# Optimization experiments

Measured on AMD Instinct MI355X. Metric: run time of the kernel, lower is better.

Reference implementation:

```python
import jax, jax.numpy as jnp
import numpy as np
from jax import lax

IN_CH, FEAT, EMB, P = 384, 256, 32, 64
OUT_CH = (256, 512, 1024, 1024)
EPS_BN = 1e-5


def _conv(x, w, b, stride=1, pad=1, groups=1):
    # x: (B,C,H,W), w: (O, C//groups, kh, kw) torch OIHW layout
    y = lax.conv_general_dilated(x, w, (stride, stride), ((pad, pad), (pad, pad)),
                                 dimension_numbers=('NCHW', 'OIHW', 'NCHW'),
                                 feature_group_count=groups)
    return y + b[None, :, None, None]


def _bn(x, g, b, m, v):
    scale = (g / jnp.sqrt(v + EPS_BN))[None, :, None, None]
    return (x - m[None, :, None, None]) * scale + b[None, :, None, None]


def _convT_block(x, w, b, k):
    # ConvTranspose2d with kernel_size == stride == k, padding 0 (non-overlapping)
    # w: (C_in, C_out, k, k) torch layout
    B, C, H, W = x.shape
    O = w.shape[1]
    y = jnp.einsum('bchw,coij->bohiwj', x, w).reshape(B, O, H * k, W * k)
    return y + b[None, :, None, None]


def _resize_ac(x, oh, ow):
    # bilinear interpolation, align_corners=True; x: (B,C,H,W)
    H, W = x.shape[-2], x.shape[-1]
    def idx(n_in, n_out):
        c = jnp.arange(n_out, dtype=x.dtype) * ((n_in - 1) / max(n_out - 1, 1))
        i0 = jnp.clip(jnp.floor(c).astype(jnp.int32), 0, max(n_in - 2, 0))
        return i0, c - i0.astype(x.dtype)
    if oh != H:
        i0, t = idx(H, oh)
        x = x[:, :, i0, :] * (1.0 - t)[:, None] + x[:, :, jnp.minimum(i0 + 1, H - 1), :] * t[:, None]
    if ow != W:
        j0, t = idx(W, ow)
        x = x[:, :, :, j0] * (1.0 - t) + x[:, :, :, jnp.minimum(j0 + 1, W - 1)] * t
    return x


def _avg3(x):
    # F.avg_pool2d(k=3, s=1, p=1) with count_include_pad=True -> always /9
    s = lax.reduce_window(x, jnp.float32(0.0), lax.add, (1, 1, 3, 3), (1, 1, 1, 1),
                          ((0, 0), (0, 0), (1, 1), (1, 1)))
    return s / 9.0


def _forward(tokens0, tokens1, tokens2, tokens3,
             proj_w0, proj_b0, proj_w1, proj_b1, proj_w2, proj_b2, proj_w3, proj_b3,
             up_w0, up_b0, up_w1, up_b1, down_w3, down_b3,
             fuse_w, fuse_b,
             pe_w1, pe_b1, pe_bn_g, pe_bn_b, pe_bn_m, pe_bn_v, pe_w2, pe_b2,
             prototypes, prototype_biases, bias_scale,
             smooth_w, smooth_b,
             head_w1, head_b1, hbn1_g, hbn1_b, hbn1_m, hbn1_v,
             head_w2, head_b2, hbn2_g, hbn2_b, hbn2_m, hbn2_v,
             head_w3, head_b3, residual_scale,
             patch_h, patch_w):
    B = tokens0.shape[0]
    toks = (tokens0, tokens1, tokens2, tokens3)
    proj = ((proj_w0, proj_b0), (proj_w1, proj_b1), (proj_w2, proj_b2), (proj_w3, proj_b3))
    feats = []
    for t, (w, b) in zip(toks, proj):
        x = t.transpose(0, 2, 1).reshape(B, t.shape[-1], patch_h, patch_w)
        x = jnp.einsum('bchw,oc->bohw', x, w[:, :, 0, 0]) + b[None, :, None, None]  # 1x1 proj
        feats.append(x)
    f0 = _convT_block(feats[0], up_w0, up_b0, 4)
    f1 = _convT_block(feats[1], up_w1, up_b1, 2)
    f2 = feats[2]                                         # identity
    f3 = _conv(feats[3], down_w3, down_b3, stride=2)
    th, tw = f0.shape[-2], f0.shape[-1]
    fused = jnp.concatenate([f0, _resize_ac(f1, th, tw), _resize_ac(f2, th, tw), _resize_ac(f3, th, tw)], axis=1)
    path1 = jax.nn.relu(jnp.einsum('bchw,oc->bohw', fused, fuse_w[:, :, 0, 0]) + fuse_b[None, :, None, None])
    H, W = patch_h * 14, patch_w * 14
    path1 = _resize_ac(path1, H, W)
    pe = _conv(path1, pe_w1, pe_b1)
    pe = jax.nn.relu(_bn(pe, pe_bn_g, pe_bn_b, pe_bn_m, pe_bn_v))
    pe = _conv(pe, pe_w2, pe_b2)                          # (B, EMB, H, W)
    sim = jnp.einsum('behw,pe->bphw', pe, prototypes) / jnp.sqrt(jnp.float32(pe.shape[1]))
    # edge map from embedding gradients, replicate-padded
    gx = jnp.abs(pe[:, :, :, :-1] - pe[:, :, :, 1:])
    gy = jnp.abs(pe[:, :, :-1, :] - pe[:, :, 1:, :])
    gx = jnp.concatenate([gx, gx[:, :, :, -1:]], axis=3)
    gy = jnp.concatenate([gy, gy[:, :, -1:, :]], axis=2)
    edge = (gx.mean(axis=1, keepdims=True) + gy.mean(axis=1, keepdims=True)) * 0.5
    mask = (edge > edge.mean()).astype(pe.dtype)
    for _ in range(2):  # fixed 2-step edge-aware smoothing
        sim = mask * sim + (1.0 - mask) * _avg3(sim)
    # first softmax over prototypes -> entropy regularizer
    act1 = jax.nn.softmax(sim, axis=1)
    activation_entropy = -(act1 * jnp.log(act1 + 1e-8)).sum(axis=1).mean()
    # spatial smoothing conv then second softmax over prototypes
    sim = _conv(sim, smooth_w, smooth_b)
    act = jax.nn.softmax(sim, axis=1)                     # (B, P, H, W)
    bb = 1.0 + jnp.tanh(prototype_biases) * bias_scale    # (P,)
    base_biases = jnp.broadcast_to(bb[None, :], (B, bb.shape[0]))
    base_gain = jnp.einsum('bphw,p->bhw', act, bb)[:, None]  # (B,1,H,W)
    # 64 per-prototype residual heads == grouped convs with groups=P
    n_proto = act.shape[1]
    h = jax.nn.relu(_bn(_conv(act, head_w1, head_b1, groups=n_proto), hbn1_g, hbn1_b, hbn1_m, hbn1_v))
    h = jax.nn.relu(_bn(_conv(h, head_w2, head_b2, groups=n_proto), hbn2_g, hbn2_b, hbn2_m, hbn2_v))
    res = _conv(h, head_w3, head_b3, groups=n_proto)      # (B, P, H, W)
    weighted = (act * res).sum(axis=1, keepdims=True)
    gain = base_gain * (1.0 + jnp.tanh(weighted) * residual_scale)
    instance_bias_map = jnp.clip(gain, 0.5, 2.0)
    return instance_bias_map, act, base_biases, weighted, pe, activation_entropy


def setup_inputs() -> dict:
    key = jax.random.key(0)
    B, N, PH, PW = 2, 256, 16, 16
    ks = iter(jax.random.split(key, 48))
    def rnd(shape, s=1.0):
        return jax.random.normal(next(ks), shape, dtype=jnp.float32) * s
    inp = {}
    for i in range(4):
        inp['tokens%d' % i] = rnd((B, N, IN_CH))
    for i, oc in enumerate(OUT_CH):
        inp['proj_w%d' % i] = rnd((oc, IN_CH, 1, 1), 0.02)
        inp['proj_b%d' % i] = rnd((oc,), 0.01)
    inp['up_w0'] = rnd((OUT_CH[0], OUT_CH[0], 4, 4), 0.02)
    inp['up_b0'] = rnd((OUT_CH[0],), 0.01)
    inp['up_w1'] = rnd((OUT_CH[1], OUT_CH[1], 2, 2), 0.02)
    inp['up_b1'] = rnd((OUT_CH[1],), 0.01)
    inp['down_w3'] = rnd((OUT_CH[3], OUT_CH[3], 3, 3), 0.01)
    inp['down_b3'] = rnd((OUT_CH[3],), 0.01)
    inp['fuse_w'] = rnd((FEAT, sum(OUT_CH), 1, 1), 0.01)
    inp['fuse_b'] = rnd((FEAT,), 0.01)
    inp['pe_w1'] = rnd((FEAT // 2, FEAT, 3, 3), 0.02)
    inp['pe_b1'] = rnd((FEAT // 2,), 0.01)
    inp['pe_bn_g'] = 1.0 + rnd((FEAT // 2,), 0.1)
    inp['pe_bn_b'] = rnd((FEAT // 2,), 0.01)
    inp['pe_bn_m'] = rnd((FEAT // 2,), 0.01)
    inp['pe_bn_v'] = jnp.ones((FEAT // 2,), jnp.float32)
    inp['pe_w2'] = rnd((EMB, FEAT // 2, 3, 3), 0.02)
    inp['pe_b2'] = rnd((EMB,), 0.01)
    inp['prototypes'] = rnd((P, EMB), 0.01)
    inp['prototype_biases'] = rnd((P,), 0.1)
    inp['bias_scale'] = jnp.asarray(0.2, jnp.float32)
    inp['smooth_w'] = rnd((P, P, 3, 3), 0.02)
    inp['smooth_b'] = rnd((P,), 0.01)
    inp['head_w1'] = rnd((P * 8, 1, 3, 3), 0.1)
    inp['head_b1'] = rnd((P * 8,), 0.01)
    inp['hbn1_g'] = 1.0 + rnd((P * 8,), 0.1)
    inp['hbn1_b'] = rnd((P * 8,), 0.01)
    inp['hbn1_m'] = rnd((P * 8,), 0.01)
    inp['hbn1_v'] = jnp.ones((P * 8,), jnp.float32)
    inp['head_w2'] = rnd((P * 8, 8, 3, 3), 0.1)
    inp['head_b2'] = rnd((P * 8,), 0.01)
    inp['hbn2_g'] = 1.0 + rnd((P * 8,), 0.1)
    inp['hbn2_b'] = rnd((P * 8,), 0.01)
    inp['hbn2_m'] = rnd((P * 8,), 0.01)
    inp['hbn2_v'] = jnp.ones((P * 8,), jnp.float32)
    inp['head_w3'] = rnd((P, 8, 3, 3), 0.1)
    inp['head_b3'] = rnd((P,), 0.01)
    inp['residual_scale'] = jnp.asarray(0.1, jnp.float32)
    inp['patch_h'] = PH
    inp['patch_w'] = PW
    return inp


def reference(tokens0, tokens1, tokens2, tokens3,
              proj_w0, proj_b0, proj_w1, proj_b1, proj_w2, proj_b2, proj_w3, proj_b3,
              up_w0, up_b0, up_w1, up_b1, down_w3, down_b3,
              fuse_w, fuse_b,
              pe_w1, pe_b1, pe_bn_g, pe_bn_b, pe_bn_m, pe_bn_v, pe_w2, pe_b2,
              prototypes, prototype_biases, bias_scale,
              smooth_w, smooth_b,
              head_w1, head_b1, hbn1_g, hbn1_b, hbn1_m, hbn1_v,
              head_w2, head_b2, hbn2_g, hbn2_b, hbn2_m, hbn2_v,
              head_w3, head_b3, residual_scale,
              patch_h, patch_w):
    return _forward(tokens0, tokens1, tokens2, tokens3,
                    proj_w0, proj_b0, proj_w1, proj_b1, proj_w2, proj_b2, proj_w3, proj_b3,
                    up_w0, up_b0, up_w1, up_b1, down_w3, down_b3,
                    fuse_w, fuse_b,
                    pe_w1, pe_b1, pe_bn_g, pe_bn_b, pe_bn_m, pe_bn_v, pe_w2, pe_b2,
                    prototypes, prototype_biases, bias_scale,
                    smooth_w, smooth_b,
                    head_w1, head_b1, hbn1_g, hbn1_b, hbn1_m, hbn1_v,
                    head_w2, head_b2, hbn2_g, hbn2_b, hbn2_m, hbn2_v,
                    head_w3, head_b3, residual_scale,
                    patch_h, patch_w)
```

## Files before the change

kernel.cpp:

```cpp
#include <hip/hip_runtime.h>
#include <math.h>

#define BATCH 2
#define NTOK 256
#define INCH 384
#define NP 50176
#define HW 224
#define NPROTO 64
#define EMBD 32

#define OFF_FEATS0   0u
#define OFF_FEATS1   131072u
#define OFF_FEATS2   393216u
#define OFF_FEATS3   917504u
#define OFF_TOKT     1441792u
#define OFF_F0       2228224u
#define OFF_F1       4325376u
#define OFF_F3       5373952u
#define OFF_FUSEDBF  5505024u
#define OFF_WD       5505024u
#define OFF_PART     14942208u
#define OFF_P64C     28573696u
#define OFF_P224C    0u
#define OFF_T1       25690112u
#define OFF_PC2      0u
#define OFF_PSM      25690112u
#define OFF_SIMA     0u
#define OFF_SIMB     6422528u
#define OFF_EDGE     12845056u
#define OFF_RES      13000000u
#define OFF_WB       13000000u
#define OFF_SHIFT    13200000u
#define OFF_BGAIN    19422528u
#define OFF_BB       19522880u
#define OFF_ACC      19523008u
#define OFF_WF       19523072u
#define OFF_WFUSE    20000000u
#define OFF_WCV0     20500000u
#define OFF_WCV1     21600000u
#define OFF_WC2      22700000u
#define OFF_WSM      22750000u

#define O_IBM 0u
#define O_ACT 100352u
#define O_BB  6522880u
#define O_WT  6523008u
#define O_PE  6623360u
#define O_ENT 9834624u

typedef __attribute__((ext_vector_type(8))) short bf16x8;
typedef __attribute__((ext_vector_type(4))) float f32x4;
typedef __attribute__((ext_vector_type(2))) float f32x2;

__device__ __forceinline__ short f2bf(float f) {
    unsigned u = __float_as_uint(f);
    unsigned r = (u + 0x7fffu + ((u >> 16) & 1u)) >> 16;
    return (short)r;
}
__device__ __forceinline__ float bf2f(short s) {
    return __uint_as_float(((unsigned)(unsigned short)s) << 16);
}

__global__ void k_transpose(const float* __restrict__ in, float* __restrict__ out) {
    int idx = blockIdx.x * 256 + threadIdx.x;
    int n = idx & 255;
    int c = (idx >> 8) % INCH;
    int b = idx / (INCH * NTOK);
    out[idx] = in[(size_t)b * INCH * NTOK + (size_t)n * INCH + c];
}

__global__ __launch_bounds__(256) void k_proj(const float* __restrict__ A,
                                              const float* __restrict__ W,
                                              const float* __restrict__ bias,
                                              float* __restrict__ out, int O) {
    int p = threadIdx.x;
    int o = blockIdx.x, b = blockIdx.y;
    const float* a = A + (size_t)b * INCH * NTOK + p;
    const float* w = W + (size_t)o * INCH;
    float acc = bias[o];
    for (int c = 0; c < INCH; ++c) acc = fmaf(a[(size_t)c * NTOK], w[c], acc);
    out[((size_t)b * O + o) * NTOK + p] = acc;
}

template <int NT>
__global__ __launch_bounds__(256) void k_wcvprep(const float* __restrict__ W,
                                                 float* __restrict__ WP, int C, int M) {
    __shared__ float t[32][33];
    int c0 = blockIdx.x * 32, m0 = blockIdx.y * 32;
    int tx = threadIdx.x & 31, ty = threadIdx.x >> 5;
#pragma unroll
    for (int r = 0; r < 4; ++r) {
        int cl = ty + r * 8;
        t[cl][tx] = W[(size_t)(c0 + cl) * M + m0 + tx];
    }
    __syncthreads();
    for (int i = threadIdx.x; i < 1024; i += 256) {
        int ml = i % NT;
        int tmp = i / NT;
        int cl = tmp & 31;
        int mh = tmp >> 5;
        WP[(size_t)(m0 / NT + mh) * C * NT + (size_t)(c0 + cl) * NT + ml] = t[cl][mh * NT + ml];
    }
}

template <int NT, int CCH, int K>
__global__ __launch_bounds__(256) void k_convt2(const float* __restrict__ X,
                                                const float* __restrict__ WP,
                                                const float* __restrict__ bias,
                                                float* __restrict__ out,
                                                int C, int O) {
    __shared__ float sX[CCH * 256];
    int tid = threadIdx.x;
    int nt = blockIdx.x, b = blockIdx.y;
    float acc[NT];
#pragma unroll
    for (int j = 0; j < NT; ++j) acc[j] = 0.f;
    const float* Xb = X + (size_t)b * C * 256;
    for (int cc = 0; cc < C; cc += CCH) {
        __syncthreads();
        const f32x4* Xg4 = (const f32x4*)(Xb + (size_t)cc * 256);
        f32x4* s4 = (f32x4*)sX;
        for (int i = tid; i < CCH * 64; i += 256) s4[i] = Xg4[i];
        __syncthreads();
        const float* wr = WP + ((size_t)nt * C + cc) * NT;
        for (int c = 0; c < CCH; ++c) {
            float xv = sX[c * 256 + tid];
            const float* w = wr + c * NT;
#pragma unroll
            for (int j = 0; j < NT; ++j) acc[j] = fmaf(xv, w[j], acc[j]);
        }
    }
    int h = tid >> 4, w = tid & 15;
    int S = 16 * K;
#pragma unroll
    for (int j = 0; j < NT; ++j) {
        int m = nt * NT + j;
        int o = m / (K * K);
        int ij = m - o * (K * K);
        int ii = ij / K, jj = ij - ii * K;
        out[((size_t)b * O + o) * (size_t)(S * S) + (h * K + ii) * S + (w * K + jj)] =
            acc[j] + bias[o];
    }
}

__global__ __launch_bounds__(256) void k_wdprep(const float* __restrict__ W,
                                                float* __restrict__ WP) {
    __shared__ float t[32][33];
    int k0 = blockIdx.x * 32, o0 = blockIdx.y * 32;
    int tx = threadIdx.x & 31, ty = threadIdx.x >> 5;
#pragma unroll
    for (int r = 0; r < 4; ++r) {
        int orow = ty + r * 8;
        t[orow][tx] = W[(size_t)(o0 + orow) * 9216 + k0 + tx];
    }
    __syncthreads();
#pragma unroll
    for (int r = 0; r < 4; ++r) {
        int krow = ty + r * 8;
        int o = o0 + tx;
        WP[(size_t)(o >> 6) * 589824 + (size_t)(k0 + krow) * 64 + (o & 63)] = t[tx][krow];
    }
}

__global__ __launch_bounds__(256) void k_down2(const float* __restrict__ X,
                                               const float* __restrict__ WP,
                                               float* __restrict__ part) {
    __shared__ float sX[64 * 256];
    int tid = threadIdx.x;
    int ot = blockIdx.x, kc = blockIdx.y, b = blockIdx.z;
    int c0 = kc * 64;
    const float* Xg = X + ((size_t)b * 1024 + c0) * 256;
    for (int i = tid; i < 16384; i += 256) {
        int c = i >> 8, px = i & 255;
        int sy = px >> 4, sx = px & 15;
        int par = (sy & 1) * 2 + (sx & 1);
        sX[(c * 4 + par) * 64 + (sy >> 1) * 8 + (sx >> 1)] = Xg[i];
    }
    __syncthreads();
    int lane = tid & 63;
    int w = __builtin_amdgcn_readfirstlane(tid >> 6);
    int oh = lane >> 3, ow = lane & 7;
    int loff[9]; float lmsk[9];
#pragma unroll
    for (int kh = 0; kh < 3; ++kh)
#pragma unroll
        for (int kw = 0; kw < 3; ++kw) {
            int py = (kh == 1) ? 0 : 1;
            int pxp = (kw == 1) ? 0 : 1;
            int u = oh - ((kh == 0) ? 1 : 0);
            int v = ow - ((kw == 0) ? 1 : 0);
            float m = (u >= 0 && v >= 0) ? 1.f : 0.f;
            if (u < 0) u = 0;
            if (v < 0) v = 0;
            loff[kh * 3 + kw] = (py * 2 + pxp) * 64 + u * 8 + v;
            lmsk[kh * 3 + kw] = m;
        }
    float acc[16];
#pragma unroll
    for (int j = 0; j < 16; ++j) acc[j] = 0.f;
    const float* wb = WP + (size_t)ot * 589824 + (size_t)c0 * 576 + w * 16;
    for (int c = 0; c < 64; ++c) {
        const float* xb = sX + c * 256;
        const float* wc = wb + (size_t)c * 576;
#pragma unroll
        for (int tap = 0; tap < 9; ++tap) {
            float xv = xb[loff[tap]] * lmsk[tap];
            const float* wr = wc + tap * 64;
#pragma unroll
            for (int j = 0; j < 16; ++j) acc[j] = fmaf(xv, wr[j], acc[j]);
        }
    }
    float* pp = part + ((size_t)((kc * 2 + b) * 1024 + ot * 64 + w * 16)) * 64 + lane;
#pragma unroll
    for (int j = 0; j < 16; ++j) pp[(size_t)j * 64] = acc[j];
}

__global__ __launch_bounds__(256) void k_downred(const float* __restrict__ part,
                                                 const float* __restrict__ bias,
                                                 float* __restrict__ out) {
    int idx = blockIdx.x * 256 + threadIdx.x;
    int o = (idx >> 6) & 1023;
    int b = idx >> 16;
    int px = idx & 63;
    float s = bias[o];
#pragma unroll
    for (int kcs = 0; kcs < 16; ++kcs)
        s += part[((size_t)(kcs * 2 + b) * 1024 + o) * 64 + px];
    out[idx] = s;
}

__global__ void k_fusedcat_bf(const float* __restrict__ f0, const float* __restrict__ f1,
                              const float* __restrict__ f2, const float* __restrict__ f3,
                              short* __restrict__ out) {
    int idx = blockIdx.x * 256 + threadIdx.x;
    int ch = idx % 2816;
    int t = idx / 2816;
    int pos = t & 4095;
    int b = t >> 12;
    float v;
    if (ch < 256) {
        v = f0[((size_t)(b * 256 + ch)) * 4096 + pos];
    } else {
        const float* src; int sh;
        if (ch < 768)       { src = f1 + ((size_t)(b * 512 + (ch - 256))) * 1024; sh = 32; }
        else if (ch < 1792) { src = f2 + ((size_t)(b * 1024 + (ch - 768))) * 256; sh = 16; }
        else                { src = f3 + ((size_t)(b * 1024 + (ch - 1792))) * 64; sh = 8;  }
        int y = pos >> 6, x = pos & 63;
        float r = (float)(sh - 1) / 63.0f;
        float cy = y * r, cx = x * r;
        int i0 = (int)cy; if (i0 > sh - 2) i0 = sh - 2;
        int j0 = (int)cx; if (j0 > sh - 2) j0 = sh - 2;
        float ty = cy - (float)i0, tx = cx - (float)j0;
        const float* s0 = src + i0 * sh + j0;
        float v00 = s0[0], v01 = s0[1], v10 = s0[sh], v11 = s0[sh + 1];
        float c0 = v00 + ty * (v10 - v00);
        float c1 = v01 + ty * (v11 - v01);
        v = c0 + tx * (c1 - c0);
    }
    out[idx] = f2bf(v);
}

__global__ void k_wfuseprep(const float* __restrict__ w, short* __restrict__ wb) {
    int idx = blockIdx.x * 256 + threadIdx.x;
    int j = idx & 7;
    int lane = (idx >> 3) & 63;
    int ntile = (idx >> 9) & 15;
    int chunk = idx >> 13;
    int oc = ntile * 16 + (lane & 15);
    int c = chunk * 32 + (lane >> 4) * 8 + j;
    wb[idx] = f2bf(w[(size_t)oc * 2816 + c]);
}

__global__ __launch_bounds__(256) void k_fuse_mfma(const short* __restrict__ A,
                                                   const bf16x8* __restrict__ WB,
                                                   const float* __restrict__ bias,
                                                   short* __restrict__ out) {
    int tid = threadIdx.x;
    int lane = tid & 63, w = tid >> 6;
    int row0 = blockIdx.x * 16;
    int l15 = lane & 15, q = lane >> 4;
    int arow = row0 + l15;
    f32x4 acc[4];
#pragma unroll
    for (int nn = 0; nn < 4; ++nn) acc[nn] = (f32x4){0.f, 0.f, 0.f, 0.f};
    const short* arp = A + (size_t)arow * 2816 + q * 8;
    for (int chunk = 0; chunk < 88; ++chunk) {
        bf16x8 a = *(const bf16x8*)(arp + chunk * 32);
        const bf16x8* wbp = WB + ((size_t)(chunk * 16 + w * 4) * 64) + lane;
#pragma unroll
        for (int nn = 0; nn < 4; ++nn) {
            bf16x8 bf = wbp[nn * 64];
            acc[nn] = __builtin_amdgcn_mfma_f32_16x16x32_bf16(a, bf, acc[nn], 0, 0, 0);
        }
    }
#pragma unroll
    for (int nn = 0; nn < 4; ++nn) {
        int oc = (w * 4 + nn) * 16 + l15;
        float bs = bias[oc];
#pragma unroll
        for (int r = 0; r < 4; ++r) {
            int m = q * 4 + r;
            out[(size_t)(row0 + m) * 256 + oc] = f2bf(fmaxf(acc[nn][r] + bs, 0.f));
        }
    }
}

__global__ void k_resize224bf2(const short* __restrict__ in, short* __restrict__ out) {
    int idx = blockIdx.x * 256 + threadIdx.x;
    int c8 = (idx & 31) * 8;
    int p = idx >> 5;
    int b = p / NP;
    int pos = p - b * NP;
    int y = pos / HW, x = pos - y * HW;
    const float r = (float)(63.0 / 223.0);
    float cy = y * r, cx = x * r;
    int i0 = (int)cy; if (i0 > 62) i0 = 62;
    int j0 = (int)cx; if (j0 > 62) j0 = 62;
    float ty = cy - (float)i0, tx = cx - (float)j0;
    const short* base = in + ((size_t)b * 4096) * 256 + c8;
    const bf16x8 v00 = *(const bf16x8*)(base + (size_t)(i0 * 64 + j0) * 256);
    const bf16x8 v01 = *(const bf16x8*)(base + (size_t)(i0 * 64 + j0 + 1) * 256);
    const bf16x8 v10 = *(const bf16x8*)(base + (size_t)((i0 + 1) * 64 + j0) * 256);
    const bf16x8 v11 = *(const bf16x8*)(base + (size_t)((i0 + 1) * 64 + j0 + 1) * 256);
    bf16x8 o;
#pragma unroll
    for (int k = 0; k < 8; ++k) {
        float a00 = bf2f(v00[k]), a01 = bf2f(v01[k]);
        float a10 = bf2f(v10[k]), a11 = bf2f(v11[k]);
        float c0 = a00 + ty * (a10 - a00);
        float c1 = a01 + ty * (a11 - a01);
        o[k] = f2bf(c0 + tx * (c1 - c0));
    }
    *(bf16x8*)(out + ((size_t)b * NP + pos) * 256 + c8) = o;
}

__global__ void k_w1prep(const float* __restrict__ w, const float* __restrict__ bias,
                         const float* __restrict__ g, const float* __restrict__ bb,
                         const float* __restrict__ m, const float* __restrict__ v,
                         short* __restrict__ wb, float* __restrict__ shift) {
    int idx = blockIdx.x * 256 + threadIdx.x;
    int j = idx & 7;
    int lane = (idx >> 3) & 63;
    int nt = (idx >> 9) & 7;
    int tc = idx >> 12;
    int tap = tc % 9, chunk = tc / 9;
    int oc = nt * 16 + (lane & 15);
    int c = chunk * 32 + (lane >> 4) * 8 + j;
    float s = g[oc] * rsqrtf(v[oc] + 1e-5f);
    wb[idx] = f2bf(w[((size_t)oc * 256 + c) * 9 + tap] * s);
    if (idx < 128) {
        float si = g[idx] * rsqrtf(v[idx] + 1e-5f);
        shift[idx] = (bias[idx] - m[idx]) * si + bb[idx];
    }
}

__global__ __launch_bounds__(256) void k_conv1mfma(const short* __restrict__ X,
                                                   const bf16x8* __restrict__ WB,
                                                   const float* __restrict__ shift,
                                                   float* __restrict__ out) {
    int tid = threadIdx.x;
    int lane = tid & 63, w = tid >> 6;
    int t = blockIdx.x;
    int b = blockIdx.y;
    int ty0 = (t / 28) * 16, tx0 = (t % 28) * 8;
    int l15 = lane & 15, q = lane >> 4;
    int loc0 = w * 32 + l15;
    int loc1 = loc0 + 16;
    int py0 = ty0 + (loc0 >> 3), px0 = tx0 + (loc0 & 7);
    int py1 = ty0 + (loc1 >> 3), px1 = tx0 + (loc1 & 7);
    int csub = q * 8;
    f32x4 acc0[8], acc1[8];
#pragma unroll
    for (int nt = 0; nt < 8; ++nt) {
        acc0[nt] = (f32x4){0.f, 0.f, 0.f, 0.f};
        acc1[nt] = (f32x4){0.f, 0.f, 0.f, 0.f};
    }
    const short* Xb = X + (size_t)b * NP * 256;
    const bf16x8 zv = {0, 0, 0, 0, 0, 0, 0, 0};
    for (int chunk = 0; chunk < 8; ++chunk) {
        int c0 = chunk * 32 + csub;
#pragma unroll
        for (int tap = 0; tap < 9; ++tap) {
            int dy = tap / 3 - 1, dx = tap % 3 - 1;
            int sy0 = py0 + dy, sx0 = px0 + dx;
            int sy1 = py1 + dy, sx1 = px1 + dx;
            bf16x8 a0 = zv, a1 = zv;
            if ((unsigned)sy0 < HW && (unsigned)sx0 < HW)
                a0 = *(const bf16x8*)(Xb + ((size_t)sy0 * HW + sx0) * 256 + c0);
            if ((unsigned)sy1 < HW && (unsigned)sx1 < HW)
                a1 = *(const bf16x8*)(Xb + ((size_t)sy1 * HW + sx1) * 256 + c0);
            const bf16x8* wbp = WB + (size_t)((chunk * 9 + tap) * 8) * 64 + lane;
#pragma unroll
            for (int nt = 0; nt < 8; ++nt) {
                bf16x8 bf = wbp[nt * 64];
                acc0[nt] = __builtin_amdgcn_mfma_f32_16x16x32_bf16(a0, bf, acc0[nt], 0, 0, 0);
                acc1[nt] = __builtin_amdgcn_mfma_f32_16x16x32_bf16(a1, bf, acc1[nt], 0, 0, 0);
            }
        }
    }
    int m0 = w * 32, m1 = w * 32 + 16;
#pragma unroll
    for (int nt = 0; nt < 8; ++nt) {
        int oc = nt * 16 + l15;
        float sh = shift[oc];
        float* ob = out + ((size_t)(b * 128 + oc)) * NP;
#pragma unroll
        for (int r = 0; r < 4; ++r) {
            int md = q * 4 + r;
            int lm = m0 + md;
            int py = ty0 + (lm >> 3), px = tx0 + (lm & 7);
            ob[py * HW + px] = fmaxf(acc0[nt][r] + sh, 0.f);
            lm = m1 + md;
            py = ty0 + (lm >> 3); px = tx0 + (lm & 7);
            ob[py * HW + px] = fmaxf(acc1[nt][r] + sh, 0.f);
        }
    }
}

__global__ void k_wc3prep(const float* __restrict__ W, float* __restrict__ WP,
                          int C, int O) {
    int idx = blockIdx.x * 256 + threadIdx.x;
    if (idx >= C * 9 * O) return;
    int o = idx % O;
    int t = idx / O;
    int tap = t % 9, c = t / 9;
    WP[idx] = W[((size_t)o * C + c) * 9 + tap];
}

template <int O, int CB>
__global__ __launch_bounds__(256) void k_conv3v3(const float* __restrict__ in,
                                                 const float* __restrict__ WP,
                                                 float* __restrict__ part, int C) {
    __shared__ float sX[8 * 360];
    int tid = threadIdx.x;
    int tb = blockIdx.x, s = blockIdx.y, b = blockIdx.z;
    int ty0 = (tb / 7) * 8, tx0 = (tb % 7) * 32;
    int px = tid & 31, py = tid >> 5;
    float acc[O];
#pragma unroll
    for (int o = 0; o < O; ++o) acc[o] = 0.f;
    int c0 = s * CB;
    const float* ic = in + ((size_t)b * C + c0) * NP;
    const float* wbase = WP + (size_t)c0 * 9 * O;
    for (int cc = 0; cc < CB; cc += 8) {
        __syncthreads();
        for (int i = tid; i < 8 * 340; i += 256) {
            int c = i / 340;
            int r = i - c * 340;
            int y = r / 34, x = r - y * 34;
            int sy = ty0 + y - 1, sx = tx0 + x - 1;
            float v = 0.f;
            if ((unsigned)sy < HW && (unsigned)sx < HW)
                v = ic[(size_t)(cc + c) * NP + sy * HW + sx];
            sX[c * 360 + y * 36 + x] = v;
        }
        __syncthreads();
        const float* xb = sX + py * 36 + px;
#pragma unroll 1
        for (int c = 0; c < 8; ++c) {
            const float* xc = xb + c * 360;
            const float* wc = wbase + (size_t)(cc + c) * 9 * O;
#pragma unroll
            for (int kh = 0; kh < 3; ++kh)
#pragma unroll
                for (int kw = 0; kw < 3; ++kw) {
                    float xv = xc[kh * 36 + kw];
                    const float* wt = wc + (kh * 3 + kw) * O;
#pragma unroll
                    for (int o = 0; o < O; ++o) acc[o] = fmaf(xv, wt[o], acc[o]);
                }
        }
    }
    int gy = ty0 + py, gx = tx0 + px;
    float* ob = part + ((size_t)(s * BATCH + b) * O) * NP + (size_t)gy * HW + gx;
#pragma unroll
    for (int o = 0; o < O; ++o) ob[(size_t)o * NP] = acc[o];
}

template <int O, int NS>
__global__ __launch_bounds__(256) void k_conv3red(const float* __restrict__ part,
                                                  const float* __restrict__ bias,
                                                  float* __restrict__ out) {
    int idx = blockIdx.x * 256 + threadIdx.x;
    int o = (idx / NP) % O;
    float v = bias[o];
#pragma unroll
    for (int s2 = 0; s2 < NS; ++s2)
        v += part[(size_t)idx + (size_t)s2 * (BATCH * O * NP)];
    out[idx] = v;
}

__global__ __launch_bounds__(256) void k_sim(const float* __restrict__ pe,
                                             const float* __restrict__ proto,
                                             float* __restrict__ sim) {
    int idx = blockIdx.x * 256 + threadIdx.x;
    int b = idx / NP, pos = idx - b * NP;
    const float* p = pe + (size_t)b * EMBD * NP + pos;
    float v[EMBD];
#pragma unroll
    for (int e = 0; e < EMBD; ++e) v[e] = p[(size_t)e * NP];
    const float scale = 1.0f / sqrtf(32.0f);
    float* so = sim + (size_t)b * NPROTO * NP + pos;
    for (int q = 0; q < NPROTO; ++q) {
        float acc = 0.f;
#pragma unroll
        for (int e = 0; e < EMBD; ++e) acc = fmaf(v[e], proto[q * EMBD + e], acc);
        so[(size_t)q * NP] = acc * scale;
    }
}

__global__ void k_init(float* acc) { if (threadIdx.x < 8) acc[threadIdx.x] = 0.f; }

__device__ __forceinline__ float block_reduce_sum(float v) {
    __shared__ float sh[4];
#pragma unroll
    for (int off = 32; off > 0; off >>= 1) v += __shfl_down(v, off);
    int lane = threadIdx.x & 63, wv = threadIdx.x >> 6;
    if (lane == 0) sh[wv] = v;
    __syncthreads();
    return (threadIdx.x == 0) ? (sh[0] + sh[1] + sh[2] + sh[3]) : 0.f;
}

__global__ __launch_bounds__(256) void k_edge(const float* __restrict__ pe,
                                              float* __restrict__ edge,
                                              float* __restrict__ acc) {
    int idx = blockIdx.x * 256 + threadIdx.x;
    int b = idx / NP, pos = idx - b * NP;
    int h = pos / HW, w = pos - h * HW;
    int wn = (w < HW - 1) ? w : HW - 2;
    int hn = (h < HW - 1) ? h : HW - 2;
    const float* pb = pe + (size_t)b * EMBD * NP;
    float sx = 0.f, sy = 0.f;
#pragma unroll 4
    for (int e = 0; e < EMBD; ++e) {
        const float* p = pb + (size_t)e * NP;
        sx += fabsf(p[h * HW + wn] - p[h * HW + wn + 1]);
        sy += fabsf(p[hn * HW + w] - p[hn * HW + HW + w]);
    }
    float ev = (sx + sy) * (0.5f / 32.0f);
    edge[idx] = ev;
    float tot = block_reduce_sum(ev);
    if (threadIdx.x == 0) atomicAdd(acc, tot);
}

__global__ void k_smooth(const float* __restrict__ sin_, const float* __restrict__ edge,
                         const float* __restrict__ acc, float* __restrict__ sout) {
    int idx = blockIdx.x * 256 + threadIdx.x;
    int pos = idx % NP;
    int bp = idx / NP;
    int b = bp >> 6;
    int h = pos / HW, w = pos - h * HW;
    float mean = acc[0] * (1.0f / 100352.0f);
    float m = (edge[(size_t)b * NP + pos] > mean) ? 1.f : 0.f;
    const float* sc = sin_ + (size_t)bp * NP;
    float s = 0.f;
#pragma unroll
    for (int dy = -1; dy <= 1; ++dy) {
        int yy = h + dy;
        if (yy < 0 || yy >= HW) continue;
#pragma unroll
        for (int dx = -1; dx <= 1; ++dx) {
            int xx = w + dx;
            if (xx < 0 || xx >= HW) continue;
            s += sc[yy * HW + xx];
        }
    }
    float c = sc[pos];
    sout[idx] = m * c + (1.f - m) * (s * (1.0f / 9.0f));
}

__global__ __launch_bounds__(256) void k_entropy(const float* __restrict__ sim,
                                                 float* __restrict__ acc) {
    int idx = blockIdx.x * 256 + threadIdx.x;
    int b = idx / NP, pos = idx - b * NP;
    const float* s = sim + (size_t)b * NPROTO * NP + pos;
    float v[NPROTO];
    float mx = -3.0e38f;
#pragma unroll
    for (int q = 0; q < NPROTO; ++q) { v[q] = s[(size_t)q * NP]; mx = fmaxf(mx, v[q]); }
    float sum = 0.f;
#pragma unroll
    for (int q = 0; q < NPROTO; ++q) { float e = expf(v[q] - mx); v[q] = e; sum += e; }
    float inv = 1.f / sum;
    float ent = 0.f;
#pragma unroll
    for (int q = 0; q < NPROTO; ++q) {
        float a = v[q] * inv;
        ent -= a * logf(a + 1e-8f);
    }
    float tot = block_reduce_sum(ent);
    if (threadIdx.x == 0) atomicAdd(acc + 1, tot);
}

__global__ void k_bb(const float* __restrict__ pb, const float* __restrict__ bs,
                     float* __restrict__ bbuf, float* __restrict__ obb) {
    int t = threadIdx.x;
    if (t < NPROTO) {
        float v = 1.f + tanhf(pb[t]) * bs[0];
        bbuf[t] = v;
        obb[t] = v;
        obb[NPROTO + t] = v;
    }
}

__global__ __launch_bounds__(256) void k_actsm(const float* __restrict__ sim,
                                               const float* __restrict__ bb,
                                               float* __restrict__ act,
                                               float* __restrict__ bgain) {
    int idx = blockIdx.x * 256 + threadIdx.x;
    int b = idx / NP, pos = idx - b * NP;
    const float* s = sim + (size_t)b * NPROTO * NP + pos;
    float v[NPROTO];
    float mx = -3.0e38f;
#pragma unroll
    for (int q = 0; q < NPROTO; ++q) { v[q] = s[(size_t)q * NP]; mx = fmaxf(mx, v[q]); }
    float sum = 0.f;
#pragma unroll
    for (int q = 0; q < NPROTO; ++q) { float e = expf(v[q] - mx); v[q] = e; sum += e; }
    float inv = 1.f / sum;
    float* a = act + (size_t)b * NPROTO * NP + pos;
    float bg = 0.f;
#pragma unroll
    for (int q = 0; q < NPROTO; ++q) {
        float p = v[q] * inv;
        a[(size_t)q * NP] = p;
        bg = fmaf(p, bb[q], bg);
    }
    bgain[idx] = bg;
}

__global__ void k_headprep(const float* __restrict__ w1, const float* __restrict__ b1,
                           const float* __restrict__ g1, const float* __restrict__ be1,
                           const float* __restrict__ m1, const float* __restrict__ v1,
                           const float* __restrict__ w2, const float* __restrict__ b2,
                           const float* __restrict__ g2, const float* __restrict__ be2,
                           const float* __restrict__ m2, const float* __restrict__ v2,
                           float* __restrict__ wf) {
    int oc = blockIdx.x * 256 + threadIdx.x;
    if (oc >= 512) return;
    float s1 = g1[oc] * rsqrtf(v1[oc] + 1e-5f);
#pragma unroll
    for (int k = 0; k < 9; ++k) wf[oc * 9 + k] = w1[oc * 9 + k] * s1;
    wf[41472 + oc] = (b1[oc] - m1[oc]) * s1 + be1[oc];
    float s2 = g2[oc] * rsqrtf(v2[oc] + 1e-5f);
    int g = oc >> 3, j = oc & 7;
#pragma unroll
    for (int icc = 0; icc < 8; ++icc)
#pragma unroll
        for (int k = 0; k < 9; ++k)
            wf[4608 + (size_t)g * 576 + icc * 72 + j * 9 + k] = w2[((size_t)oc * 8 + icc) * 9 + k] * s2;
    wf[41984 + oc] = (b2[oc] - m2[oc]) * s2 + be2[oc];
}

__global__ __launch_bounds__(256) void k_heads(
    const float* __restrict__ act, const float* __restrict__ wf,
    const float* __restrict__ w3, const float* __restrict__ b3,
    float* __restrict__ res) {
    __shared__ float sA[22 * 24];
    __shared__ float sH1[8][20 * 22];
    __shared__ float sH2[8][18 * 18];
    int tid = threadIdx.x;
    int tile = blockIdx.x, g = blockIdx.y, b = blockIdx.z;
    int oy0 = (tile / 14) * 16, ox0 = (tile % 14) * 16;
    const float* ain = act + (size_t)(b * NPROTO + g) * NP;

    for (int i = tid; i < 484; i += 256) {
        int y = i / 22, x = i - y * 22;
        int gy = oy0 - 3 + y, gx = ox0 - 3 + x;
        float v = 0.f;
        if ((unsigned)gy < HW && (unsigned)gx < HW) v = ain[gy * HW + gx];
        sA[y * 24 + x] = v;
    }
    __syncthreads();

    const float* b1f = wf + 41472 + g * 8;
    for (int i = tid; i < 400; i += 256) {
        int y = i / 20, x = i - y * 20;
        int gy = oy0 - 2 + y, gx = ox0 - 2 + x;
        float keep = ((unsigned)gy < HW && (unsigned)gx < HW) ? 1.f : 0.f;
        const float* s0 = sA + y * 24 + x;
        float r0 = s0[0],  r1 = s0[1],  r2 = s0[2];
        float r3 = s0[24], r4 = s0[25], r5 = s0[26];
        float r6 = s0[48], r7 = s0[49], r8 = s0[50];
#pragma unroll
        for (int j = 0; j < 8; ++j) {
            const float* w = wf + (g * 8 + j) * 9;
            float v = fmaf(r0, w[0], fmaf(r1, w[1], fmaf(r2, w[2],
                      fmaf(r3, w[3], fmaf(r4, w[4], fmaf(r5, w[5],
                      fmaf(r6, w[6], fmaf(r7, w[7], fmaf(r8, w[8], b1f[j])))))))));
            sH1[j][y * 22 + x] = fmaxf(v, 0.f) * keep;
        }
    }
    __syncthreads();

    const float* w2f = wf + 4608 + (size_t)g * 576;
    const float* b2f = wf + 41984 + g * 8;
    if (tid < 162) {
        int y2 = tid / 9, xp = (tid - y2 * 9) * 2;
        f32x2 a2[8];
#pragma unroll
        for (int j = 0; j < 8; ++j) { float bv = b2f[j]; a2[j] = (f32x2){bv, bv}; }
#pragma unroll
        for (int icc = 0; icc < 8; ++icc) {
            const float* s0 = &sH1[icc][y2 * 22 + xp];
            f32x2 t[9];
#pragma unroll
            for (int r = 0; r < 3; ++r) {
                float f0 = s0[r * 22], f1 = s0[r * 22 + 1];
                float f2 = s0[r * 22 + 2], f3 = s0[r * 22 + 3];
                t[r * 3 + 0] = (f32x2){f0, f1};
                t[r * 3 + 1] = (f32x2){f1, f2};
                t[r * 3 + 2] = (f32x2){f2, f3};
            }
            const float* wr = w2f + icc * 72;
#pragma unroll
            for (int j = 0; j < 8; ++j) {
                const float* wj = wr + j * 9;
#pragma unroll
                for (int k = 0; k < 9; ++k) {
                    float wv = wj[k];
                    a2[j] = __builtin_elementwise_fma(t[k], (f32x2){wv, wv}, a2[j]);
                }
            }
        }
        int gy = oy0 - 1 + y2;
        int gx0 = ox0 - 1 + xp;
        float k0 = ((unsigned)gy < HW && (unsigned)gx0 < HW) ? 1.f : 0.f;
        float k1 = ((unsigned)gy < HW && (unsigned)(gx0 + 1) < HW) ? 1.f : 0.f;
        f32x2 kp = (f32x2){k0, k1};
        const f32x2 z2 = (f32x2){0.f, 0.f};
#pragma unroll
        for (int j = 0; j < 8; ++j) {
            f32x2 v = __builtin_elementwise_max(a2[j], z2) * kp;
            sH2[j][y2 * 18 + xp] = v.x;
            sH2[j][y2 * 18 + xp + 1] = v.y;
        }
    }
    __syncthreads();

    if (tid < 128) {
        int y3 = tid >> 3, xp = (tid & 7) * 2;
        float bv = b3[g];
        f32x2 a2 = (f32x2){bv, bv};
#pragma unroll
        for (int icc = 0; icc < 8; ++icc) {
            const float* s0 = &sH2[icc][y3 * 18 + xp];
            const float* w = w3 + (size_t)(g * 8 + icc) * 9;
#pragma unroll
            for (int r = 0; r < 3; ++r) {
                float f0 = s0[r * 18], f1 = s0[r * 18 + 1];
                float f2 = s0[r * 18 + 2], f3 = s0[r * 18 + 3];
                float w0 = w[r * 3], w1 = w[r * 3 + 1], w2v = w[r * 3 + 2];
                a2 = __builtin_elementwise_fma((f32x2){f0, f1}, (f32x2){w0, w0}, a2);
                a2 = __builtin_elementwise_fma((f32x2){f1, f2}, (f32x2){w1, w1}, a2);
                a2 = __builtin_elementwise_fma((f32x2){f2, f3}, (f32x2){w2v, w2v}, a2);
            }
        }
        float* rp = res + (size_t)(b * NPROTO + g) * NP + (size_t)(oy0 + y3) * HW + (ox0 + xp);
        rp[0] = a2.x;
        rp[1] = a2.y;
    }
}

__global__ __launch_bounds__(256) void k_final(const float* __restrict__ act,
                                               const float* __restrict__ res,
                                               const float* __restrict__ bgain,
                                               const float* __restrict__ rscale,
                                               float* __restrict__ owt,
                                               float* __restrict__ oibm) {
    int idx = blockIdx.x * 256 + threadIdx.x;
    int b = idx / NP, pos = idx - b * NP;
    const float* a = act + (size_t)b * NPROTO * NP + pos;
    const float* r = res + (size_t)b * NPROTO * NP + pos;
    float wt = 0.f;
#pragma unroll
    for (int q = 0; q < NPROTO; ++q) wt = fmaf(a[(size_t)q * NP], r[(size_t)q * NP], wt);
    owt[idx] = wt;
    float gn = bgain[idx] * (1.f + tanhf(wt) * rscale[0]);
    gn = fminf(fmaxf(gn, 0.5f), 2.0f);
    oibm[idx] = gn;
}

__global__ void k_entfinal(const float* __restrict__ acc, float* __restrict__ o) {
    if (threadIdx.x == 0) o[0] = acc[1] * (1.0f / 100352.0f);
}

extern "C" void kernel_launch(void* const* d_in, const int* in_sizes, int n_in,
                              void* d_out, int out_size, void* d_ws, size_t ws_size,
                              hipStream_t stream) {
    const float* tokens[4] = {(const float*)d_in[0], (const float*)d_in[1],
                              (const float*)d_in[2], (const float*)d_in[3]};
    const float* proj_w[4] = {(const float*)d_in[4], (const float*)d_in[6],
                              (const float*)d_in[8], (const float*)d_in[10]};
    const float* proj_b[4] = {(const float*)d_in[5], (const float*)d_in[7],
                              (const float*)d_in[9], (const float*)d_in[11]};
    const float* up_w0 = (const float*)d_in[12]; const float* up_b0 = (const float*)d_in[13];
    const float* up_w1 = (const float*)d_in[14]; const float* up_b1 = (const float*)d_in[15];
    const float* down_w3 = (const float*)d_in[16]; const float* down_b3 = (const float*)d_in[17];
    const float* fuse_w = (const float*)d_in[18]; const float* fuse_b = (const float*)d_in[19];
    const float* pe_w1 = (const float*)d_in[20]; const float* pe_b1 = (const float*)d_in[21];
    const float* pe_bn_g = (const float*)d_in[22]; const float* pe_bn_b = (const float*)d_in[23];
    const float* pe_bn_m = (const float*)d_in[24]; const float* pe_bn_v = (const float*)d_in[25];
    const float* pe_w2 = (const float*)d_in[26]; const float* pe_b2 = (const float*)d_in[27];
    const float* prototypes = (const float*)d_in[28];
    const float* proto_biases = (const float*)d_in[29];
    const float* bias_scale = (const float*)d_in[30];
    const float* smooth_w = (const float*)d_in[31]; const float* smooth_b = (const float*)d_in[32];
    const float* hw1 = (const float*)d_in[33]; const float* hb1 = (const float*)d_in[34];
    const float* hg1 = (const float*)d_in[35]; const float* hbe1 = (const float*)d_in[36];
    const float* hm1 = (const float*)d_in[37]; const float* hv1 = (const float*)d_in[38];
    const float* hw2 = (const float*)d_in[39]; const float* hb2 = (const float*)d_in[40];
    const float* hg2 = (const float*)d_in[41]; const float* hbe2 = (const float*)d_in[42];
    const float* hm2 = (const float*)d_in[43]; const float* hv2 = (const float*)d_in[44];
    const float* hw3 = (const float*)d_in[45]; const float* hb3 = (const float*)d_in[46];
    const float* rscale = (const float*)d_in[47];
    (void)in_sizes; (void)n_in; (void)out_size; (void)ws_size;

    float* ws = (float*)d_ws;
    float* FEATS[4] = {ws + OFF_FEATS0, ws + OFF_FEATS1, ws + OFF_FEATS2, ws + OFF_FEATS3};
    float* TOKT = ws + OFF_TOKT;
    float* F0 = ws + OFF_F0; float* F1 = ws + OFF_F1; float* F3 = ws + OFF_F3;
    short* FUSEDBF = (short*)(ws + OFF_FUSEDBF);
    short* P64C = (short*)(ws + OFF_P64C);
    short* P224C = (short*)(ws + OFF_P224C);
    short* WB = (short*)(ws + OFF_WB);
    short* WFUSE = (short*)(ws + OFF_WFUSE);
    float* SHIFT = ws + OFF_SHIFT;
    float* T1 = ws + OFF_T1;
    float* SIMA = ws + OFF_SIMA; float* SIMB = ws + OFF_SIMB;
    float* EDGE = ws + OFF_EDGE; float* RES = ws + OFF_RES;
    float* BGAIN = ws + OFF_BGAIN; float* BBUF = ws + OFF_BB; float* ACC = ws + OFF_ACC;
    float* WF = ws + OFF_WF;
    float* WDP = ws + OFF_WD;
    float* PART = ws + OFF_PART;
    float* WCV0 = ws + OFF_WCV0;
    float* WCV1 = ws + OFF_WCV1;
    float* WC2 = ws + OFF_WC2;
    float* WSM = ws + OFF_WSM;
    float* PC2 = ws + OFF_PC2;
    float* PSM = ws + OFF_PSM;

    float* out = (float*)d_out;
    float* o_ibm = out + O_IBM; float* o_act = out + O_ACT; float* o_bb = out + O_BB;
    float* o_wt = out + O_WT; float* o_pe = out + O_PE; float* o_ent = out + O_ENT;

    const int OCH[4] = {256, 512, 1024, 1024};
    for (int s = 0; s < 4; ++s)
        k_transpose<<<768, 256, 0, stream>>>(tokens[s], TOKT + s * 196608);
    for (int s = 0; s < 4; ++s)
        k_proj<<<dim3(OCH[s], BATCH), 256, 0, stream>>>(TOKT + s * 196608, proj_w[s], proj_b[s],
                                                        FEATS[s], OCH[s]);
    k_wcvprep<16><<<dim3(8, 128), 256, 0, stream>>>(up_w0, WCV0, 256, 4096);
    k_wcvprep<8><<<dim3(16, 64), 256, 0, stream>>>(up_w1, WCV1, 512, 2048);
    k_convt2<16, 64, 4><<<dim3(256, BATCH), 256, 0, stream>>>(FEATS[0], WCV0, up_b0, F0, 256, 256);
    k_convt2<8, 64, 2><<<dim3(256, BATCH), 256, 0, stream>>>(FEATS[1], WCV1, up_b1, F1, 512, 512);
    k_wdprep<<<dim3(288, 32), 256, 0, stream>>>(down_w3, WDP);
    k_down2<<<dim3(16, 16, BATCH), 256, 0, stream>>>(FEATS[3], WDP, PART);
    k_downred<<<512, 256, 0, stream>>>(PART, down_b3, F3);
    k_wc3prep<<<144, 256, 0, stream>>>(pe_w2, WC2, 128, 32);
    k_wc3prep<<<144, 256, 0, stream>>>(smooth_w, WSM, 64, 64);
    k_wfuseprep<<<2816, 256, 0, stream>>>(fuse_w, WFUSE);
    k_fusedcat_bf<<<90112, 256, 0, stream>>>(F0, F1, FEATS[2], F3, FUSEDBF);
    k_fuse_mfma<<<512, 256, 0, stream>>>(FUSEDBF, (const bf16x8*)WFUSE, fuse_b, P64C);
    k_w1prep<<<1152, 256, 0, stream>>>(pe_w1, pe_b1, pe_bn_g, pe_bn_b, pe_bn_m, pe_bn_v,
                                       WB, SHIFT);
    k_resize224bf2<<<12544, 256, 0, stream>>>(P64C, P224C);
    k_conv1mfma<<<dim3(392, BATCH), 256, 0, stream>>>(P224C, (const bf16x8*)WB, SHIFT, T1);
    k_conv3v3<32, 32><<<dim3(196, 4, BATCH), 256, 0, stream>>>(T1, WC2, PC2, 128);
    k_conv3red<32, 4><<<12544, 256, 0, stream>>>(PC2, pe_b2, o_pe);
    k_sim<<<392, 256, 0, stream>>>(o_pe, prototypes, SIMA);
    k_init<<<1, 64, 0, stream>>>(ACC);
    k_edge<<<392, 256, 0, stream>>>(o_pe, EDGE, ACC);
    k_smooth<<<25088, 256, 0, stream>>>(SIMA, EDGE, ACC, SIMB);
    k_smooth<<<25088, 256, 0, stream>>>(SIMB, EDGE, ACC, SIMA);
    k_entropy<<<392, 256, 0, stream>>>(SIMA, ACC);
    k_conv3v3<64, 32><<<dim3(196, 2, BATCH), 256, 0, stream>>>(SIMA, WSM, PSM, 64);
    k_conv3red<64, 2><<<25088, 256, 0, stream>>>(PSM, smooth_b, SIMB);
    k_bb<<<1, 64, 0, stream>>>(proto_biases, bias_scale, BBUF, o_bb);
    k_actsm<<<392, 256, 0, stream>>>(SIMB, BBUF, o_act, BGAIN);
    k_headprep<<<2, 256, 0, stream>>>(hw1, hb1, hg1, hbe1, hm1, hv1,
                                      hw2, hb2, hg2, hbe2, hm2, hv2, WF);
    k_heads<<<dim3(196, 64, BATCH), 256, 0, stream>>>(o_act, WF, hw3, hb3, RES);
    k_final<<<392, 256, 0, stream>>>(o_act, RES, BGAIN, rscale, o_wt, o_ibm);
    k_entfinal<<<1, 1, 0, stream>>>(ACC, o_ent);
}
```

Before: 1.582 ms.

## Fuse conv partial reductions into consumers and two smoothing passes into one tiled kernel

Folds the split-K partial sum reduction for the embedding conv into the prototype similarity kernel. It also folds the smoothing-conv reduction into the softmax/activation kernel, so both separate reduce kernels go away. The two successive edge-masked 3x3 average smoothing passes become one shared-memory tiled kernel that computes the intermediate with a halo. This removes several full-size global memory round trips and kernel launches. The cost is redundant halo computation and more register pressure in the fused kernels.

```diff
diff --git a/kernel.cpp b/kernel.cpp
--- a/kernel.cpp
+++ b/kernel.cpp
@@ -24,6 +24,7 @@
 #define OFF_P224C    0u
 #define OFF_T1       25690112u
 #define OFF_PC2      0u
+#define OFF_SIMRAW   25690112u
 #define OFF_PSM      25690112u
 #define OFF_SIMA     0u
 #define OFF_SIMB     6422528u
@@ -477,34 +478,29 @@
     for (int o = 0; o < O; ++o) ob[(size_t)o * NP] = acc[o];
 }
 
-template <int O, int NS>
-__global__ __launch_bounds__(256) void k_conv3red(const float* __restrict__ part,
+__global__ __launch_bounds__(256) void k_red32sim(const float* __restrict__ part,
                                                   const float* __restrict__ bias,
-                                                  float* __restrict__ out) {
-    int idx = blockIdx.x * 256 + threadIdx.x;
-    int o = (idx / NP) % O;
-    float v = bias[o];
-#pragma unroll
-    for (int s2 = 0; s2 < NS; ++s2)
-        v += part[(size_t)idx + (size_t)s2 * (BATCH * O * NP)];
-    out[idx] = v;
-}
-
-__global__ __launch_bounds__(256) void k_sim(const float* __restrict__ pe,
-                                             const float* __restrict__ proto,
-                                             float* __restrict__ sim) {
+                                                  const float* __restrict__ proto,
+                                                  float* __restrict__ o_pe,
+                                                  float* __restrict__ simout) {
     int idx = blockIdx.x * 256 + threadIdx.x;
     int b = idx / NP, pos = idx - b * NP;
-    const float* p = pe + (size_t)b * EMBD * NP + pos;
-    float v[EMBD];
-#pragma unroll
-    for (int e = 0; e < EMBD; ++e) v[e] = p[(size_t)e * NP];
+    float v[32];
+#pragma unroll
+    for (int o = 0; o < 32; ++o) {
+        float s = bias[o];
+#pragma unroll
+        for (int s2 = 0; s2 < 4; ++s2)
+            s += part[((size_t)((s2 * BATCH + b) * 32 + o)) * NP + pos];
+        v[o] = s;
+        o_pe[((size_t)(b * 32 + o)) * NP + pos] = s;
+    }
     const float scale = 1.0f / sqrtf(32.0f);
-    float* so = sim + (size_t)b * NPROTO * NP + pos;
+    float* so = simout + (size_t)b * NPROTO * NP + pos;
     for (int q = 0; q < NPROTO; ++q) {
         float acc = 0.f;
 #pragma unroll
-        for (int e = 0; e < EMBD; ++e) acc = fmaf(v[e], proto[q * EMBD + e], acc);
+        for (int e = 0; e < 32; ++e) acc = fmaf(v[e], proto[q * EMBD + e], acc);
         so[(size_t)q * NP] = acc * scale;
     }
 }
@@ -543,30 +539,60 @@
     if (threadIdx.x == 0) atomicAdd(acc, tot);
 }
 
-__global__ void k_smooth(const float* __restrict__ sin_, const float* __restrict__ edge,
-                         const float* __restrict__ acc, float* __restrict__ sout) {
-    int idx = blockIdx.x * 256 + threadIdx.x;
-    int pos = idx % NP;
-    int bp = idx / NP;
-    int b = bp >> 6;
-    int h = pos / HW, w = pos - h * HW;
+__global__ __launch_bounds__(256) void k_smooth2x(const float* __restrict__ sin_,
+                                                  const float* __restrict__ edge,
+                                                  const float* __restrict__ acc,
+                                                  float* __restrict__ sout) {
+    __shared__ float sIn[20 * 20];
+    __shared__ float sE[18 * 18];
+    __shared__ float s1[18 * 18];
+    int tid = threadIdx.x;
+    int tile = blockIdx.x, p = blockIdx.y, b = blockIdx.z;
+    int oy0 = (tile / 14) * 16, ox0 = (tile % 14) * 16;
     float mean = acc[0] * (1.0f / 100352.0f);
-    float m = (edge[(size_t)b * NP + pos] > mean) ? 1.f : 0.f;
-    const float* sc = sin_ + (size_t)bp * NP;
-    float s = 0.f;
-#pragma unroll
-    for (int dy = -1; dy <= 1; ++dy) {
-        int yy = h + dy;
-        if (yy < 0 || yy >= HW) continue;
-#pragma unroll
-        for (int dx = -1; dx <= 1; ++dx) {
-            int xx = w + dx;
-            if (xx < 0 || xx >= HW) continue;
-            s += sc[yy * HW + xx];
-        }
-    }
-    float c = sc[pos];
-    sout[idx] = m * c + (1.f - m) * (s * (1.0f / 9.0f));
+    const float* sc = sin_ + ((size_t)(b * NPROTO + p)) * NP;
+    const float* eb = edge + (size_t)b * NP;
+    for (int i = tid; i < 400; i += 256) {
+        int y = i / 20, x = i - y * 20;
+        int gy = oy0 - 2 + y, gx = ox0 - 2 + x;
+        float v = 0.f;
+        if ((unsigned)gy < HW && (unsigned)gx < HW) v = sc[gy * HW + gx];
+        sIn[i] = v;
+    }
+    for (int i = tid; i < 324; i += 256) {
+        int y = i / 18, x = i - y * 18;
+        int gy = oy0 - 1 + y, gx = ox0 - 1 + x;
+        float e = 0.f;
+        if ((unsigned)gy < HW && (unsigned)gx < HW) e = eb[gy * HW + gx];
+        sE[i] = e;
+    }
+    __syncthreads();
+    for (int i = tid; i < 324; i += 256) {
+        int y = i / 18, x = i - y * 18;
+        int gy = oy0 - 1 + y, gx = ox0 - 1 + x;
+        float r = 0.f;
+        if ((unsigned)gy < HW && (unsigned)gx < HW) {
+            const float* c0 = sIn + (y + 1) * 20 + (x + 1);
+            float s = c0[-21] + c0[-20] + c0[-19]
+                    + c0[-1]  + c0[0]   + c0[1]
+                    + c0[19]  + c0[20]  + c0[21];
+            float m = (sE[i] > mean) ? 1.f : 0.f;
+            r = m * c0[0] + (1.f - m) * (s * (1.0f / 9.0f));
+        }
+        s1[i] = r;
+    }
+    __syncthreads();
+    {
+        int px = tid & 15, py = tid >> 4;
+        int gy = oy0 + py, gx = ox0 + px;
+        const float* c1 = s1 + (py + 1) * 18 + (px + 1);
+        float s = c1[-19] + c1[-18] + c1[-17]
+                + c1[-1]  + c1[0]   + c1[1]
+                + c1[17]  + c1[18]  + c1[19];
+        float m = (sE[(py + 1) * 18 + (px + 1)] > mean) ? 1.f : 0.f;
+        sout[((size_t)(b * NPROTO + p)) * NP + (size_t)gy * HW + gx] =
+            m * c1[0] + (1.f - m) * (s * (1.0f / 9.0f));
+    }
 }
 
 __global__ __launch_bounds__(256) void k_entropy(const float* __restrict__ sim,
@@ -603,17 +629,23 @@
     }
 }
 
-__global__ __launch_bounds__(256) void k_actsm(const float* __restrict__ sim,
-                                               const float* __restrict__ bb,
-                                               float* __restrict__ act,
-                                               float* __restrict__ bgain) {
+__global__ __launch_bounds__(256) void k_actsm2(const float* __restrict__ part,
+                                                const float* __restrict__ bias,
+                                                const float* __restrict__ bb,
+                                                float* __restrict__ act,
+                                                float* __restrict__ bgain) {
     int idx = blockIdx.x * 256 + threadIdx.x;
     int b = idx / NP, pos = idx - b * NP;
-    const float* s = sim + (size_t)b * NPROTO * NP + pos;
     float v[NPROTO];
     float mx = -3.0e38f;
 #pragma unroll
-    for (int q = 0; q < NPROTO; ++q) { v[q] = s[(size_t)q * NP]; mx = fmaxf(mx, v[q]); }
+    for (int q = 0; q < NPROTO; ++q) {
+        float s = bias[q];
+        s += part[((size_t)((0 * BATCH + b) * NPROTO + q)) * NP + pos];
+        s += part[((size_t)((1 * BATCH + b) * NPROTO + q)) * NP + pos];
+        v[q] = s;
+        mx = fmaxf(mx, s);
+    }
     float sum = 0.f;
 #pragma unroll
     for (int q = 0; q < NPROTO; ++q) { float e = expf(v[q] - mx); v[q] = e; sum += e; }
@@ -827,7 +859,8 @@
     short* WFUSE = (short*)(ws + OFF_WFUSE);
     float* SHIFT = ws + OFF_SHIFT;
     float* T1 = ws + OFF_T1;
-    float* SIMA = ws + OFF_SIMA; float* SIMB = ws + OFF_SIMB;
+    float* SIMA = ws + OFF_SIMA;
+    float* SIMRAW = ws + OFF_SIMRAW;
     float* EDGE = ws + OFF_EDGE; float* RES = ws + OFF_RES;
     float* BGAIN = ws + OFF_BGAIN; float* BBUF = ws + OFF_BB; float* ACC = ws + OFF_ACC;
     float* WF = ws + OFF_WF;
@@ -867,17 +900,14 @@
     k_resize224bf2<<<12544, 256, 0, stream>>>(P64C, P224C);
     k_conv1mfma<<<dim3(392, BATCH), 256, 0, stream>>>(P224C, (const bf16x8*)WB, SHIFT, T1);
     k_conv3v3<32, 32><<<dim3(196, 4, BATCH), 256, 0, stream>>>(T1, WC2, PC2, 128);
-    k_conv3red<32, 4><<<12544, 256, 0, stream>>>(PC2, pe_b2, o_pe);
-    k_sim<<<392, 256, 0, stream>>>(o_pe, prototypes, SIMA);
+    k_red32sim<<<392, 256, 0, stream>>>(PC2, pe_b2, prototypes, o_pe, SIMRAW);
     k_init<<<1, 64, 0, stream>>>(ACC);
     k_edge<<<392, 256, 0, stream>>>(o_pe, EDGE, ACC);
-    k_smooth<<<25088, 256, 0, stream>>>(SIMA, EDGE, ACC, SIMB);
-    k_smooth<<<25088, 256, 0, stream>>>(SIMB, EDGE, ACC, SIMA);
+    k_smooth2x<<<dim3(196, NPROTO, BATCH), 256, 0, stream>>>(SIMRAW, EDGE, ACC, SIMA);
     k_entropy<<<392, 256, 0, stream>>>(SIMA, ACC);
     k_conv3v3<64, 32><<<dim3(196, 2, BATCH), 256, 0, stream>>>(SIMA, WSM, PSM, 64);
-    k_conv3red<64, 2><<<25088, 256, 0, stream>>>(PSM, smooth_b, SIMB);
     k_bb<<<1, 64, 0, stream>>>(proto_biases, bias_scale, BBUF, o_bb);
-    k_actsm<<<392, 256, 0, stream>>>(SIMB, BBUF, o_act, BGAIN);
+    k_actsm2<<<392, 256, 0, stream>>>(PSM, smooth_b, BBUF, o_act, BGAIN);
     k_headprep<<<2, 256, 0, stream>>>(hw1, hb1, hg1, hbe1, hm1, hv1,
                                       hw2, hb2, hg2, hbe2, hm2, hv2, WF);
     k_heads<<<dim3(196, 64, BATCH), 256, 0, stream>>>(o_act, WF, hw3, hb3, RES);
```

Result: faster. 1.534 ms (-3.0%).
